# Optimization experiments

Measured on AMD Instinct MI355X. Metric: run time of the kernel, lower is better.

## Reference

```python
import jax, jax.numpy as jnp
import numpy as np

B, H, W, C = 32, 64, 64, 256


def setup_inputs() -> dict:
    key = jax.random.key(0)
    ks = jax.random.split(key, 4)
    scale = 1.0 / np.sqrt(C)
    return {
        "x": jax.random.normal(ks[0], (B, H, W, C), dtype=jnp.float32),
        "wq": jax.random.normal(ks[1], (C, C), dtype=jnp.float32) * scale,
        "bq": jnp.zeros((C,), dtype=jnp.float32),
        "wk": jax.random.normal(ks[2], (C, C), dtype=jnp.float32) * scale,
        "bk": jnp.zeros((C,), dtype=jnp.float32),
        "wv": jax.random.normal(ks[3], (C, C), dtype=jnp.float32) * scale,
        "bv": jnp.zeros((C,), dtype=jnp.float32),
    }


def reference(x, wq, bq, wk, bk, wv, bv):
    # 1x1 convs == per-pixel dense projections
    q = jnp.einsum('bhwc,cf->bhwf', x, wq) + bq
    k = jnp.einsum('bhwc,cf->bhwf', x, wk) + bk
    v = jnp.einsum('bhwc,cf->bhwf', x, wv) + bv
    # tf.matmul(key, query, transpose_b=True): batch dims (b,h), contract over c
    attn = jnp.einsum('bhwc,bhvc->bhwv', k, q)  # [B,H,W,W], NO 1/sqrt(d) scaling
    attn = jax.nn.softmax(attn, axis=-1)
    out = jnp.einsum('bhwv,bhvc->bhwc', attn, v)  # [B,H,W,C]
    return out * x  # elementwise gate with raw input
```

## Files before the change

kernel.cpp:

```cpp
#include <hip/hip_runtime.h>

#define CD   256
#define WD   64
#define NBH  2048
#define XST  264
#define VST  72
#define SST  68

typedef unsigned short u16;
typedef __attribute__((ext_vector_type(8))) short bfrag_t;
typedef __attribute__((ext_vector_type(4))) float f4_t;

#define MFMA(a, b, c) __builtin_amdgcn_mfma_f32_16x16x32_bf16(a, b, c, 0, 0, 0)

__device__ __forceinline__ u16 f2bf(float f) {
    unsigned u = __float_as_uint(f);
    u += 0x7fffu + ((u >> 16) & 1u);
    return (u16)(u >> 16);
}
__device__ __forceinline__ float bf2f(u16 h) {
    return __uint_as_float(((unsigned)h) << 16);
}

__global__ __launch_bounds__(256) void prep_m(
    const float* __restrict__ wq, const float* __restrict__ wk,
    u16* __restrict__ Mthi, u16* __restrict__ Mtlo)
{
    __shared__ float swq[16 * 257];
    __shared__ float swk[32 * 257];
    const int t = threadIdx.x;
    const int dt = blockIdx.x >> 3;
    const int ct = blockIdx.x & 7;
    #pragma unroll
    for (int n = 0; n < 16; ++n) {
        int idx = n * 256 + t;
        int d = idx >> 8, f = idx & 255;
        swq[d * 257 + f] = wq[(dt * 16 + d) * CD + f];
    }
    #pragma unroll
    for (int n = 0; n < 32; ++n) {
        int idx = n * 256 + t;
        int c = idx >> 8, f = idx & 255;
        swk[c * 257 + f] = wk[(ct * 32 + c) * CD + f];
    }
    __syncthreads();
    const int d = t & 15, c0 = (t >> 4) * 2;
    #pragma unroll
    for (int cc = 0; cc < 2; ++cc) {
        const float* kr = &swk[(c0 + cc) * 257];
        const float* qr = &swq[d * 257];
        float acc = 0.f;
        #pragma unroll 8
        for (int f = 0; f < CD; ++f) acc = fmaf(kr[f], qr[f], acc);
        u16 h = f2bf(acc);
        int off = (dt * 16 + d) * CD + ct * 32 + c0 + cc;
        Mthi[off] = h;
        Mtlo[off] = f2bf(acc - bf2f(h));
    }
}

__global__ __launch_bounds__(256) void prep_v(
    const float* __restrict__ wv, u16* __restrict__ Wvthi)
{
    __shared__ float tile[64 * 65];
    const int t = threadIdx.x;
    const int bc = blockIdx.x >> 2, bd = blockIdx.x & 3;
    #pragma unroll
    for (int n = 0; n < 16; ++n) {
        int idx = n * 256 + t;
        int c = idx >> 6, d = idx & 63;
        tile[c * 65 + d] = wv[(bc * 64 + c) * CD + bd * 64 + d];
    }
    __syncthreads();
    #pragma unroll
    for (int n = 0; n < 16; ++n) {
        int idx = n * 256 + t;
        int d = idx >> 6, c = idx & 63;
        Wvthi[(bd * 64 + d) * CD + bc * 64 + c] = f2bf(tile[c * 65 + d]);
    }
}

__global__ __launch_bounds__(256) void prep_b(
    const float* __restrict__ wq, const float* __restrict__ bk,
    float* __restrict__ wqbk)
{
    __shared__ float sbk[CD];
    const int t = threadIdx.x;
    if (t < CD) sbk[t] = bk[t];
    __syncthreads();
    const int c = blockIdx.x * 16 + (t >> 4), part = t & 15;
    const float* wr = wq + c * CD + part * 16;
    const float* br = sbk + part * 16;
    float a = 0.f;
    #pragma unroll
    for (int j = 0; j < 16; ++j) a = fmaf(wr[j], br[j], a);
    a += __shfl_xor(a, 1);
    a += __shfl_xor(a, 2);
    a += __shfl_xor(a, 4);
    a += __shfl_xor(a, 8);
    if (part == 0) wqbk[c] = a;
}

extern __shared__ char smem_raw[];

__global__ __launch_bounds__(1024, 4) void attn_kernel(
    const float* __restrict__ x,
    const u16* __restrict__ Mthi, const u16* __restrict__ Mtlo,
    const u16* __restrict__ Wvthi, const float* __restrict__ wqbk,
    const float* __restrict__ bv, float* __restrict__ out)
{
    u16* sXhi = (u16*)smem_raw;
    u16* sXlo = sXhi + WD * XST;
    u16* sThi = sXlo + WD * XST;
    u16* sTlo = sThi + WD * XST;
    u16* sVt  = sThi;
    float* sS  = (float*)(sTlo + WD * XST);
    float* sxb = sS + WD * SST;
    float* sbv = sxb + WD;

    const int t = threadIdx.x;
    const int wave = t >> 6, lane = t & 63;
    const int lane15 = lane & 15, quad = lane >> 4;
    const int bh = blockIdx.x;
    const float* __restrict__ xblk = x + (size_t)bh * (WD * CD);
    float* __restrict__ oblk = out + (size_t)bh * (WD * CD);

    if (t < CD) sbv[t] = bv[t];
    {
        const float4* xv4 = (const float4*)xblk;
        #pragma unroll
        for (int n = 0; n < 4; ++n) {
            int idx = n * 1024 + t;
            float4 v = xv4[idx];
            int i = idx >> 6;
            int c = (idx & 63) << 2;
            ushort4 h4, l4;
            h4.x = f2bf(v.x); l4.x = f2bf(v.x - bf2f(h4.x));
            h4.y = f2bf(v.y); l4.y = f2bf(v.y - bf2f(h4.y));
            h4.z = f2bf(v.z); l4.z = f2bf(v.z - bf2f(h4.z));
            h4.w = f2bf(v.w); l4.w = f2bf(v.w - bf2f(h4.w));
            *(ushort4*)&sXhi[i * XST + c] = h4;
            *(ushort4*)&sXlo[i * XST + c] = l4;
        }
    }
    {
        const int row = t >> 4, part = t & 15;
        const float* xr = xblk + row * CD + part * 16;
        const float* br = wqbk + part * 16;
        float a = 0.f;
        #pragma unroll
        for (int i = 0; i < 4; ++i) {
            float4 xv = *(const float4*)&xr[i * 4];
            float4 bvv = *(const float4*)&br[i * 4];
            a = fmaf(xv.x, bvv.x, a); a = fmaf(xv.y, bvv.y, a);
            a = fmaf(xv.z, bvv.z, a); a = fmaf(xv.w, bvv.w, a);
        }
        a += __shfl_xor(a, 1);
        a += __shfl_xor(a, 2);
        a += __shfl_xor(a, 4);
        a += __shfl_xor(a, 8);
        if (part == 0) sxb[row] = a;
    }
    __syncthreads();

    {
        f4_t acc[4];
        const f4_t z = {0.f, 0.f, 0.f, 0.f};
        #pragma unroll
        for (int a = 0; a < 4; ++a) acc[a] = z;

        const int drow = wave * 16 + lane15;
        #pragma unroll
        for (int kk = 0; kk < 8; ++kk) {
            const int k0 = kk * 32 + quad * 8;
            const int mo = drow * CD + k0;
            bfrag_t Ah = *(const bfrag_t*)(Mthi + mo);
            bfrag_t Al = *(const bfrag_t*)(Mtlo + mo);
            bfrag_t Bh[4], Bl[4];
            #pragma unroll
            for (int nt = 0; nt < 4; ++nt) {
                const int xo = (nt * 16 + lane15) * XST + k0;
                Bh[nt] = *(const bfrag_t*)(sXhi + xo);
                Bl[nt] = *(const bfrag_t*)(sXlo + xo);
            }
            #pragma unroll
            for (int nt = 0; nt < 4; ++nt) {
                acc[nt] = MFMA(Ah, Bh[nt], acc[nt]);
                acc[nt] = MFMA(Ah, Bl[nt], acc[nt]);
                acc[nt] = MFMA(Al, Bh[nt], acc[nt]);
            }
        }
        #pragma unroll
        for (int nt = 0; nt < 4; ++nt) {
            const int i  = nt * 16 + lane15;
            const int d0 = wave * 16 + quad * 4;
            ushort4 h4, l4;
            float f;
            f = acc[nt][0]; h4.x = f2bf(f); l4.x = f2bf(f - bf2f(h4.x));
            f = acc[nt][1]; h4.y = f2bf(f); l4.y = f2bf(f - bf2f(h4.y));
            f = acc[nt][2]; h4.z = f2bf(f); l4.z = f2bf(f - bf2f(h4.z));
            f = acc[nt][3]; h4.w = f2bf(f); l4.w = f2bf(f - bf2f(h4.w));
            *(ushort4*)&sThi[i * XST + d0] = h4;
            *(ushort4*)&sTlo[i * XST + d0] = l4;
        }
    }
    __syncthreads();

    {
        f4_t acc = {0.f, 0.f, 0.f, 0.f};
        const int m0 = (wave >> 2) * 16;
        const int n0 = (wave & 3) * 16;
        #pragma unroll
        for (int kk = 0; kk < 8; ++kk) {
            const int k0 = kk * 32 + quad * 8;
            const int to = (m0 + lane15) * XST + k0;
            const int xo = (n0 + lane15) * XST + k0;
            bfrag_t Th = *(const bfrag_t*)(sThi + to);
            bfrag_t Tl = *(const bfrag_t*)(sTlo + to);
            bfrag_t Xh = *(const bfrag_t*)(sXhi + xo);
            bfrag_t Xl = *(const bfrag_t*)(sXlo + xo);
            acc = MFMA(Th, Xh, acc);
            acc = MFMA(Th, Xl, acc);
            acc = MFMA(Tl, Xh, acc);
        }
        const int v = n0 + lane15;
        const float xbv = sxb[v];
        #pragma unroll
        for (int r = 0; r < 4; ++r) {
            const int wtok = m0 + quad * 4 + r;
            sS[wtok * SST + v] = acc[r] + xbv;
        }
    }
    __syncthreads();

    {
        f4_t acc[4];
        const f4_t z = {0.f, 0.f, 0.f, 0.f};
        #pragma unroll
        for (int a = 0; a < 4; ++a) acc[a] = z;

        const int drow = wave * 16 + lane15;
        #pragma unroll
        for (int kk = 0; kk < 8; ++kk) {
            const int k0 = kk * 32 + quad * 8;
            bfrag_t Af = *(const bfrag_t*)(Wvthi + drow * CD + k0);
            #pragma unroll
            for (int nt = 0; nt < 4; ++nt) {
                bfrag_t Bf = *(const bfrag_t*)(sXhi + (nt * 16 + lane15) * XST + k0);
                acc[nt] = MFMA(Af, Bf, acc[nt]);
            }
        }
        #pragma unroll
        for (int nt = 0; nt < 4; ++nt) {
            const int j = nt * 16 + lane15;
            #pragma unroll
            for (int r = 0; r < 4; ++r) {
                const int d = wave * 16 + quad * 4 + r;
                sVt[d * VST + j] = f2bf(acc[nt][r] + sbv[d]);
            }
        }
    }
    {
        const int row = t >> 4, part = t & 15;
        float* srow = &sS[row * SST + part * 4];
        float e[4];
        float mx = fmaxf(fmaxf(srow[0], srow[1]), fmaxf(srow[2], srow[3]));
        mx = fmaxf(mx, __shfl_xor(mx, 1));
        mx = fmaxf(mx, __shfl_xor(mx, 2));
        mx = fmaxf(mx, __shfl_xor(mx, 4));
        mx = fmaxf(mx, __shfl_xor(mx, 8));
        float sum = 0.f;
        #pragma unroll
        for (int u = 0; u < 4; ++u) { e[u] = __expf(srow[u] - mx); sum += e[u]; }
        sum += __shfl_xor(sum, 1);
        sum += __shfl_xor(sum, 2);
        sum += __shfl_xor(sum, 4);
        sum += __shfl_xor(sum, 8);
        float inv = 1.0f / sum;
        #pragma unroll
        for (int u = 0; u < 4; ++u) srow[u] = e[u] * inv;
    }
    __syncthreads();

    {
        f4_t acc[4];
        const f4_t z = {0.f, 0.f, 0.f, 0.f};
        #pragma unroll
        for (int a = 0; a < 4; ++a) acc[a] = z;

        const int m0 = (wave & 3) * 16;
        const int nbase = (wave >> 2) * 64;
        #pragma unroll
        for (int kk = 0; kk < 2; ++kk) {
            const int k0 = kk * 32 + quad * 8;
            const float* p = &sS[(m0 + lane15) * SST + k0];
            f4_t p0 = *(const f4_t*)p;
            f4_t p1 = *(const f4_t*)(p + 4);
            bfrag_t Af;
            Af[0] = (short)f2bf(p0[0]); Af[1] = (short)f2bf(p0[1]);
            Af[2] = (short)f2bf(p0[2]); Af[3] = (short)f2bf(p0[3]);
            Af[4] = (short)f2bf(p1[0]); Af[5] = (short)f2bf(p1[1]);
            Af[6] = (short)f2bf(p1[2]); Af[7] = (short)f2bf(p1[3]);
            #pragma unroll
            for (int nt = 0; nt < 4; ++nt) {
                bfrag_t Bf = *(const bfrag_t*)(sVt + (nbase + nt * 16 + lane15) * VST + k0);
                acc[nt] = MFMA(Af, Bf, acc[nt]);
            }
        }
        #pragma unroll
        for (int nt = 0; nt < 4; ++nt) {
            const int d = nbase + nt * 16 + lane15;
            #pragma unroll
            for (int r = 0; r < 4; ++r) {
                const int wtok = m0 + quad * 4 + r;
                float g = xblk[wtok * CD + d];
                oblk[wtok * CD + d] = acc[nt][r] * g;
            }
        }
    }
}

extern "C" void kernel_launch(void* const* d_in, const int* in_sizes, int n_in,
                              void* d_out, int out_size, void* d_ws, size_t ws_size,
                              hipStream_t stream) {
    const float* x  = (const float*)d_in[0];
    const float* wq = (const float*)d_in[1];
    const float* wk = (const float*)d_in[3];
    const float* bk = (const float*)d_in[4];
    const float* wv = (const float*)d_in[5];
    const float* bv = (const float*)d_in[6];
    float* out = (float*)d_out;

    char* ws = (char*)d_ws;
    u16* Mthi   = (u16*)ws;
    u16* Mtlo   = (u16*)(ws + (128 << 10));
    u16* Wvthi  = (u16*)(ws + (256 << 10));
    float* wqbk = (float*)(ws + (384 << 10));

    prep_m<<<128, 256, 0, stream>>>(wq, wk, Mthi, Mtlo);
    prep_v<<<16, 256, 0, stream>>>(wv, Wvthi);
    prep_b<<<16, 256, 0, stream>>>(wq, bk, wqbk);

    const size_t lds = (size_t)(4 * WD * XST * sizeof(u16)) +
                       (WD * SST + WD + CD) * sizeof(float);
    hipFuncSetAttribute((const void*)attn_kernel,
                        hipFuncAttributeMaxDynamicSharedMemorySize, (int)lds);
    attn_kernel<<<NBH, 1024, lds, stream>>>(x, Mthi, Mtlo, Wvthi, wqbk, bv, out);
}
```

Baseline: 374.6 us.

## Make attention kernel persistent and prefetch next tile's input during PV stage

The launch shrinks to 256 blocks, and each block loops over 8 (b,h) slices instead of handling one. Inside the loop, the next slice's x is loaded from global memory before the final PV MFMA stage, so that load latency overlaps compute. The converted x and its bias dot product are then written to LDS before the output store, with the bias kept in a double buffer. The score GEMM also splits its three MFMA chains into separate accumulators to break the dependency chain. The costs are fewer resident blocks per CU and more registers held live during the prefetch.

```diff
diff --git a/kernel.cpp b/kernel.cpp
--- a/kernel.cpp
+++ b/kernel.cpp
@@ -3,6 +3,8 @@
 #define CD   256
 #define WD   64
 #define NBH  2048
+#define GRID 256
+#define ITER (NBH / GRID)
 #define XST  264
 #define VST  72
 #define SST  68
@@ -114,19 +116,18 @@
     u16* sThi = sXlo + WD * XST;
     u16* sTlo = sThi + WD * XST;
     u16* sVt  = sThi;
-    float* sS  = (float*)(sTlo + WD * XST);
-    float* sxb = sS + WD * SST;
-    float* sbv = sxb + WD;
+    float* sS   = (float*)(sTlo + WD * XST);
+    float* sxb2 = sS + WD * SST;
+    float* sbv  = sxb2 + 2 * WD;
 
     const int t = threadIdx.x;
     const int wave = t >> 6, lane = t & 63;
     const int lane15 = lane & 15, quad = lane >> 4;
-    const int bh = blockIdx.x;
-    const float* __restrict__ xblk = x + (size_t)bh * (WD * CD);
-    float* __restrict__ oblk = out + (size_t)bh * (WD * CD);
 
     if (t < CD) sbv[t] = bv[t];
+
     {
+        const float* __restrict__ xblk = x + (size_t)blockIdx.x * (WD * CD);
         const float4* xv4 = (const float4*)xblk;
         #pragma unroll
         for (int n = 0; n < 4; ++n) {
@@ -142,8 +143,6 @@
             *(ushort4*)&sXhi[i * XST + c] = h4;
             *(ushort4*)&sXlo[i * XST + c] = l4;
         }
-    }
-    {
         const int row = t >> 4, part = t & 15;
         const float* xr = xblk + row * CD + part * 16;
         const float* br = wqbk + part * 16;
@@ -159,164 +158,216 @@
         a += __shfl_xor(a, 2);
         a += __shfl_xor(a, 4);
         a += __shfl_xor(a, 8);
-        if (part == 0) sxb[row] = a;
+        if (part == 0) sxb2[row] = a;
     }
     __syncthreads();
 
-    {
-        f4_t acc[4];
-        const f4_t z = {0.f, 0.f, 0.f, 0.f};
-        #pragma unroll
-        for (int a = 0; a < 4; ++a) acc[a] = z;
-
-        const int drow = wave * 16 + lane15;
-        #pragma unroll
-        for (int kk = 0; kk < 8; ++kk) {
-            const int k0 = kk * 32 + quad * 8;
-            const int mo = drow * CD + k0;
-            bfrag_t Ah = *(const bfrag_t*)(Mthi + mo);
-            bfrag_t Al = *(const bfrag_t*)(Mtlo + mo);
-            bfrag_t Bh[4], Bl[4];
+    for (int it = 0; it < ITER; ++it) {
+        const int bh = blockIdx.x + (it << 8);
+        const float* __restrict__ xblk = x + (size_t)bh * (WD * CD);
+        float* __restrict__ oblk = out + (size_t)bh * (WD * CD);
+        const float* __restrict__ xnext = x + (size_t)(bh + GRID) * (WD * CD);
+        const float* sxb_cur = sxb2 + (it & 1) * WD;
+        float* sxb_nxt = sxb2 + ((it + 1) & 1) * WD;
+
+        {
+            f4_t acc[4];
+            const f4_t z = {0.f, 0.f, 0.f, 0.f};
+            #pragma unroll
+            for (int a = 0; a < 4; ++a) acc[a] = z;
+
+            const int drow = wave * 16 + lane15;
+            #pragma unroll
+            for (int kk = 0; kk < 8; ++kk) {
+                const int k0 = kk * 32 + quad * 8;
+                const int mo = drow * CD + k0;
+                bfrag_t Ah = *(const bfrag_t*)(Mthi + mo);
+                bfrag_t Al = *(const bfrag_t*)(Mtlo + mo);
+                bfrag_t Bh[4], Bl[4];
+                #pragma unroll
+                for (int nt = 0; nt < 4; ++nt) {
+                    const int xo = (nt * 16 + lane15) * XST + k0;
+                    Bh[nt] = *(const bfrag_t*)(sXhi + xo);
+                    Bl[nt] = *(const bfrag_t*)(sXlo + xo);
+                }
+                #pragma unroll
+                for (int nt = 0; nt < 4; ++nt) {
+                    acc[nt] = MFMA(Ah, Bh[nt], acc[nt]);
+                    acc[nt] = MFMA(Ah, Bl[nt], acc[nt]);
+                    acc[nt] = MFMA(Al, Bh[nt], acc[nt]);
+                }
+            }
             #pragma unroll
             for (int nt = 0; nt < 4; ++nt) {
-                const int xo = (nt * 16 + lane15) * XST + k0;
-                Bh[nt] = *(const bfrag_t*)(sXhi + xo);
-                Bl[nt] = *(const bfrag_t*)(sXlo + xo);
-            }
-            #pragma unroll
-            for (int nt = 0; nt < 4; ++nt) {
-                acc[nt] = MFMA(Ah, Bh[nt], acc[nt]);
-                acc[nt] = MFMA(Ah, Bl[nt], acc[nt]);
-                acc[nt] = MFMA(Al, Bh[nt], acc[nt]);
-            }
-        }
-        #pragma unroll
-        for (int nt = 0; nt < 4; ++nt) {
-            const int i  = nt * 16 + lane15;
-            const int d0 = wave * 16 + quad * 4;
-            ushort4 h4, l4;
-            float f;
-            f = acc[nt][0]; h4.x = f2bf(f); l4.x = f2bf(f - bf2f(h4.x));
-            f = acc[nt][1]; h4.y = f2bf(f); l4.y = f2bf(f - bf2f(h4.y));
-            f = acc[nt][2]; h4.z = f2bf(f); l4.z = f2bf(f - bf2f(h4.z));
-            f = acc[nt][3]; h4.w = f2bf(f); l4.w = f2bf(f - bf2f(h4.w));
-            *(ushort4*)&sThi[i * XST + d0] = h4;
-            *(ushort4*)&sTlo[i * XST + d0] = l4;
-        }
-    }
-    __syncthreads();
-
-    {
-        f4_t acc = {0.f, 0.f, 0.f, 0.f};
-        const int m0 = (wave >> 2) * 16;
-        const int n0 = (wave & 3) * 16;
-        #pragma unroll
-        for (int kk = 0; kk < 8; ++kk) {
-            const int k0 = kk * 32 + quad * 8;
-            const int to = (m0 + lane15) * XST + k0;
-            const int xo = (n0 + lane15) * XST + k0;
-            bfrag_t Th = *(const bfrag_t*)(sThi + to);
-            bfrag_t Tl = *(const bfrag_t*)(sTlo + to);
-            bfrag_t Xh = *(const bfrag_t*)(sXhi + xo);
-            bfrag_t Xl = *(const bfrag_t*)(sXlo + xo);
-            acc = MFMA(Th, Xh, acc);
-            acc = MFMA(Th, Xl, acc);
-            acc = MFMA(Tl, Xh, acc);
-        }
-        const int v = n0 + lane15;
-        const float xbv = sxb[v];
-        #pragma unroll
-        for (int r = 0; r < 4; ++r) {
-            const int wtok = m0 + quad * 4 + r;
-            sS[wtok * SST + v] = acc[r] + xbv;
-        }
-    }
-    __syncthreads();
-
-    {
-        f4_t acc[4];
-        const f4_t z = {0.f, 0.f, 0.f, 0.f};
-        #pragma unroll
-        for (int a = 0; a < 4; ++a) acc[a] = z;
-
-        const int drow = wave * 16 + lane15;
-        #pragma unroll
-        for (int kk = 0; kk < 8; ++kk) {
-            const int k0 = kk * 32 + quad * 8;
-            bfrag_t Af = *(const bfrag_t*)(Wvthi + drow * CD + k0);
-            #pragma unroll
-            for (int nt = 0; nt < 4; ++nt) {
-                bfrag_t Bf = *(const bfrag_t*)(sXhi + (nt * 16 + lane15) * XST + k0);
-                acc[nt] = MFMA(Af, Bf, acc[nt]);
-            }
-        }
-        #pragma unroll
-        for (int nt = 0; nt < 4; ++nt) {
-            const int j = nt * 16 + lane15;
-            #pragma unroll
-            for (int r = 0; r < 4; ++r) {
-                const int d = wave * 16 + quad * 4 + r;
-                sVt[d * VST + j] = f2bf(acc[nt][r] + sbv[d]);
-            }
-        }
-    }
-    {
-        const int row = t >> 4, part = t & 15;
-        float* srow = &sS[row * SST + part * 4];
-        float e[4];
-        float mx = fmaxf(fmaxf(srow[0], srow[1]), fmaxf(srow[2], srow[3]));
-        mx = fmaxf(mx, __shfl_xor(mx, 1));
-        mx = fmaxf(mx, __shfl_xor(mx, 2));
-        mx = fmaxf(mx, __shfl_xor(mx, 4));
-        mx = fmaxf(mx, __shfl_xor(mx, 8));
-        float sum = 0.f;
-        #pragma unroll
-        for (int u = 0; u < 4; ++u) { e[u] = __expf(srow[u] - mx); sum += e[u]; }
-        sum += __shfl_xor(sum, 1);
-        sum += __shfl_xor(sum, 2);
-        sum += __shfl_xor(sum, 4);
-        sum += __shfl_xor(sum, 8);
-        float inv = 1.0f / sum;
-        #pragma unroll
-        for (int u = 0; u < 4; ++u) srow[u] = e[u] * inv;
-    }
-    __syncthreads();
-
-    {
-        f4_t acc[4];
-        const f4_t z = {0.f, 0.f, 0.f, 0.f};
-        #pragma unroll
-        for (int a = 0; a < 4; ++a) acc[a] = z;
-
-        const int m0 = (wave & 3) * 16;
-        const int nbase = (wave >> 2) * 64;
-        #pragma unroll
-        for (int kk = 0; kk < 2; ++kk) {
-            const int k0 = kk * 32 + quad * 8;
-            const float* p = &sS[(m0 + lane15) * SST + k0];
-            f4_t p0 = *(const f4_t*)p;
-            f4_t p1 = *(const f4_t*)(p + 4);
-            bfrag_t Af;
-            Af[0] = (short)f2bf(p0[0]); Af[1] = (short)f2bf(p0[1]);
-            Af[2] = (short)f2bf(p0[2]); Af[3] = (short)f2bf(p0[3]);
-            Af[4] = (short)f2bf(p1[0]); Af[5] = (short)f2bf(p1[1]);
-            Af[6] = (short)f2bf(p1[2]); Af[7] = (short)f2bf(p1[3]);
-            #pragma unroll
-            for (int nt = 0; nt < 4; ++nt) {
-                bfrag_t Bf = *(const bfrag_t*)(sVt + (nbase + nt * 16 + lane15) * VST + k0);
-                acc[nt] = MFMA(Af, Bf, acc[nt]);
-            }
-        }
-        #pragma unroll
-        for (int nt = 0; nt < 4; ++nt) {
-            const int d = nbase + nt * 16 + lane15;
+                const int i  = nt * 16 + lane15;
+                const int d0 = wave * 16 + quad * 4;
+                ushort4 h4, l4;
+                float f;
+                f = acc[nt][0]; h4.x = f2bf(f); l4.x = f2bf(f - bf2f(h4.x));
+                f = acc[nt][1]; h4.y = f2bf(f); l4.y = f2bf(f - bf2f(h4.y));
+                f = acc[nt][2]; h4.z = f2bf(f); l4.z = f2bf(f - bf2f(h4.z));
+                f = acc[nt][3]; h4.w = f2bf(f); l4.w = f2bf(f - bf2f(h4.w));
+                *(ushort4*)&sThi[i * XST + d0] = h4;
+                *(ushort4*)&sTlo[i * XST + d0] = l4;
+            }
+        }
+        __syncthreads();
+
+        {
+            const f4_t z = {0.f, 0.f, 0.f, 0.f};
+            f4_t a0 = z, a1 = z, a2 = z;
+            const int m0 = (wave >> 2) * 16;
+            const int n0 = (wave & 3) * 16;
+            #pragma unroll
+            for (int kk = 0; kk < 8; ++kk) {
+                const int k0 = kk * 32 + quad * 8;
+                const int to = (m0 + lane15) * XST + k0;
+                const int xo = (n0 + lane15) * XST + k0;
+                bfrag_t Th = *(const bfrag_t*)(sThi + to);
+                bfrag_t Tl = *(const bfrag_t*)(sTlo + to);
+                bfrag_t Xh = *(const bfrag_t*)(sXhi + xo);
+                bfrag_t Xl = *(const bfrag_t*)(sXlo + xo);
+                a0 = MFMA(Th, Xh, a0);
+                a1 = MFMA(Th, Xl, a1);
+                a2 = MFMA(Tl, Xh, a2);
+            }
+            const int v = n0 + lane15;
+            const float xbv = sxb_cur[v];
             #pragma unroll
             for (int r = 0; r < 4; ++r) {
                 const int wtok = m0 + quad * 4 + r;
-                float g = xblk[wtok * CD + d];
-                oblk[wtok * CD + d] = acc[nt][r] * g;
-            }
-        }
+                sS[wtok * SST + v] = a0[r] + a1[r] + a2[r] + xbv;
+            }
+        }
+        __syncthreads();
+
+        {
+            f4_t acc[4];
+            const f4_t z = {0.f, 0.f, 0.f, 0.f};
+            #pragma unroll
+            for (int a = 0; a < 4; ++a) acc[a] = z;
+
+            const int drow = wave * 16 + lane15;
+            #pragma unroll
+            for (int kk = 0; kk < 8; ++kk) {
+                const int k0 = kk * 32 + quad * 8;
+                bfrag_t Af = *(const bfrag_t*)(Wvthi + drow * CD + k0);
+                #pragma unroll
+                for (int nt = 0; nt < 4; ++nt) {
+                    bfrag_t Bf = *(const bfrag_t*)(sXhi + (nt * 16 + lane15) * XST + k0);
+                    acc[nt] = MFMA(Af, Bf, acc[nt]);
+                }
+            }
+            #pragma unroll
+            for (int nt = 0; nt < 4; ++nt) {
+                const int j = nt * 16 + lane15;
+                #pragma unroll
+                for (int r = 0; r < 4; ++r) {
+                    const int d = wave * 16 + quad * 4 + r;
+                    sVt[d * VST + j] = f2bf(acc[nt][r] + sbv[d]);
+                }
+            }
+        }
+        {
+            const int row = t >> 4, part = t & 15;
+            float* srow = &sS[row * SST + part * 4];
+            float e[4];
+            float mx = fmaxf(fmaxf(srow[0], srow[1]), fmaxf(srow[2], srow[3]));
+            mx = fmaxf(mx, __shfl_xor(mx, 1));
+            mx = fmaxf(mx, __shfl_xor(mx, 2));
+            mx = fmaxf(mx, __shfl_xor(mx, 4));
+            mx = fmaxf(mx, __shfl_xor(mx, 8));
+            float sum = 0.f;
+            #pragma unroll
+            for (int u = 0; u < 4; ++u) { e[u] = __expf(srow[u] - mx); sum += e[u]; }
+            sum += __shfl_xor(sum, 1);
+            sum += __shfl_xor(sum, 2);
+            sum += __shfl_xor(sum, 4);
+            sum += __shfl_xor(sum, 8);
+            float inv = 1.0f / sum;
+            #pragma unroll
+            for (int u = 0; u < 4; ++u) srow[u] = e[u] * inv;
+        }
+        __syncthreads();
+
+        {
+            float4 xv[4];
+            if (it + 1 < ITER) {
+                const float4* xnv4 = (const float4*)xnext;
+                #pragma unroll
+                for (int n = 0; n < 4; ++n) xv[n] = xnv4[n * 1024 + t];
+            }
+
+            f4_t acc[4];
+            const f4_t z = {0.f, 0.f, 0.f, 0.f};
+            #pragma unroll
+            for (int a = 0; a < 4; ++a) acc[a] = z;
+
+            const int m0 = (wave & 3) * 16;
+            const int nbase = (wave >> 2) * 64;
+            #pragma unroll
+            for (int kk = 0; kk < 2; ++kk) {
+                const int k0 = kk * 32 + quad * 8;
+                const float* p = &sS[(m0 + lane15) * SST + k0];
+                f4_t p0 = *(const f4_t*)p;
+                f4_t p1 = *(const f4_t*)(p + 4);
+                bfrag_t Af;
+                Af[0] = (short)f2bf(p0[0]); Af[1] = (short)f2bf(p0[1]);
+                Af[2] = (short)f2bf(p0[2]); Af[3] = (short)f2bf(p0[3]);
+                Af[4] = (short)f2bf(p1[0]); Af[5] = (short)f2bf(p1[1]);
+                Af[6] = (short)f2bf(p1[2]); Af[7] = (short)f2bf(p1[3]);
+                #pragma unroll
+                for (int nt = 0; nt < 4; ++nt) {
+                    bfrag_t Bf = *(const bfrag_t*)(sVt + (nbase + nt * 16 + lane15) * VST + k0);
+                    acc[nt] = MFMA(Af, Bf, acc[nt]);
+                }
+            }
+
+            if (it + 1 < ITER) {
+                #pragma unroll
+                for (int n = 0; n < 4; ++n) {
+                    int idx = n * 1024 + t;
+                    int i = idx >> 6;
+                    int c = (idx & 63) << 2;
+                    float4 v = xv[n];
+                    ushort4 h4, l4;
+                    h4.x = f2bf(v.x); l4.x = f2bf(v.x - bf2f(h4.x));
+                    h4.y = f2bf(v.y); l4.y = f2bf(v.y - bf2f(h4.y));
+                    h4.z = f2bf(v.z); l4.z = f2bf(v.z - bf2f(h4.z));
+                    h4.w = f2bf(v.w); l4.w = f2bf(v.w - bf2f(h4.w));
+                    *(ushort4*)&sXhi[i * XST + c] = h4;
+                    *(ushort4*)&sXlo[i * XST + c] = l4;
+                }
+                const int row = t >> 4, part = t & 15;
+                const float* xr = xnext + row * CD + part * 16;
+                const float* br = wqbk + part * 16;
+                float a = 0.f;
+                #pragma unroll
+                for (int i = 0; i < 4; ++i) {
+                    float4 xq = *(const float4*)&xr[i * 4];
+                    float4 bq = *(const float4*)&br[i * 4];
+                    a = fmaf(xq.x, bq.x, a); a = fmaf(xq.y, bq.y, a);
+                    a = fmaf(xq.z, bq.z, a); a = fmaf(xq.w, bq.w, a);
+                }
+                a += __shfl_xor(a, 1);
+                a += __shfl_xor(a, 2);
+                a += __shfl_xor(a, 4);
+                a += __shfl_xor(a, 8);
+                if (part == 0) sxb_nxt[row] = a;
+            }
+
+            #pragma unroll
+            for (int nt = 0; nt < 4; ++nt) {
+                const int d = nbase + nt * 16 + lane15;
+                #pragma unroll
+                for (int r = 0; r < 4; ++r) {
+                    const int wtok = m0 + quad * 4 + r;
+                    float g = xblk[wtok * CD + d];
+                    oblk[wtok * CD + d] = acc[nt][r] * g;
+                }
+            }
+        }
+        __syncthreads();
     }
 }
 
@@ -342,8 +393,8 @@
     prep_b<<<16, 256, 0, stream>>>(wq, bk, wqbk);
 
     const size_t lds = (size_t)(4 * WD * XST * sizeof(u16)) +
-                       (WD * SST + WD + CD) * sizeof(float);
+                       (WD * SST + 2 * WD + CD) * sizeof(float);
     hipFuncSetAttribute((const void*)attn_kernel,
                         hipFuncAttributeMaxDynamicSharedMemorySize, (int)lds);
-    attn_kernel<<<NBH, 1024, lds, stream>>>(x, Mthi, Mtlo, Wvthi, wqbk, bv, out);
-}
+    attn_kernel<<<GRID, 1024, lds, stream>>>(x, Mthi, Mtlo, Wvthi, wqbk, bv, out);
+}
```

Measured after the change: 485.8 us. +29.7%, slower.
